# Optimization experiments

Hardware: AMD Instinct MI355X
Metric: run time of the kernel (lower is better)

## Reference

```python
import jax, jax.numpy as jnp
import numpy as np

B, S, F, D, H, L = 32, 512, 40, 512, 8, 4
T = S + 1
DK, DV = D // 2, D          # expand_k=0.5, expand_v=1.0 (fla GLA defaults)
HK, HV = DK // H, DV // H
GLR = 16                    # gate low-rank dim
GLN = 16.0                  # gate logit normalizer
MLP = 4 * D


def sin_pos(t, d, n=10000.0):
    pos = jnp.arange(t, dtype=jnp.float32)[:, None]
    den = jnp.power(n, 2.0 * jnp.arange(d // 2, dtype=jnp.float32) / d)
    e = jnp.zeros((t, d), jnp.float32)
    e = e.at[:, 0::2].set(jnp.sin(pos / den))
    e = e.at[:, 1::2].set(jnp.cos(pos / den))
    return e


def layernorm(x, w, b, eps=1e-5):
    m = x.mean(-1, keepdims=True)
    v = ((x - m) ** 2).mean(-1, keepdims=True)
    return (x - m) * jax.lax.rsqrt(v + eps) * w + b


def bin_norm(x, l1, b1, l2, b2, y1, y2):
    # x: (b, f, s). BiN: temporal z-norm with per-feature affine (X2) +
    # feature z-norm with per-time affine (X1); unbiased std, small std -> 1.
    st = jnp.sqrt(x.var(axis=2, ddof=1, keepdims=True))
    st = jnp.where(st < 1e-4, 1.0, st)
    Z2 = (x - x.mean(axis=2, keepdims=True)) / st
    X2 = l2[None, :, None] * Z2 + b2[None, :, None]
    sf = jnp.sqrt(x.var(axis=1, ddof=1, keepdims=True))
    sf = jnp.where(sf < 1e-4, 1.0, sf)
    Z1 = (x - x.mean(axis=1, keepdims=True)) / sf
    X1 = l1[None, None, :] * Z1 + b1[None, None, :]
    return y1 * X1 + y2 * X2


def gla_attn(x, qw, kw, vw, gw, gkw1, gkw2, gkb2, gnw, ow):
    # Gated linear attention, recurrent form: S_t = exp(gk_t) * S_{t-1} + k_t v_t^T
    b, t, _ = x.shape
    q = (x @ qw).reshape(b, t, H, HK) * (HK ** -0.5)
    k = (x @ kw).reshape(b, t, H, HK)
    v = (x @ vw).reshape(b, t, H, HV)
    g = (x @ gw).reshape(b, t, H, HV)
    gk = (jax.nn.log_sigmoid((x @ gkw1) @ gkw2 + gkb2) / GLN).reshape(b, t, H, HK)

    def step(Sc, inp):
        qt, kt, vt, gt = inp                       # (b,H,HK),(b,H,HK),(b,H,HV),(b,H,HK)
        Sc = Sc * jnp.exp(gt)[..., None] + kt[..., None] * vt[..., None, :]
        return Sc, jnp.einsum('bhk,bhkv->bhv', qt, Sc)

    init = jnp.zeros((b, H, HK, HV), x.dtype)
    to_t = lambda a: jnp.swapaxes(a, 0, 1)        # (t, b, H, dim)
    _, o = jax.lax.scan(step, init, (to_t(q), to_t(k), to_t(v), to_t(gk)))
    o = jnp.swapaxes(o, 0, 1)                     # (b, t, H, HV)
    o = o * jax.lax.rsqrt((o * o).mean(-1, keepdims=True) + 1e-5) * gnw  # head RMSNorm
    o = o * g * jax.nn.sigmoid(g)                 # swish output gate
    return o.reshape(b, t, DV) @ ow


def setup_inputs():
    key = jax.random.key(0)
    ks = iter(jax.random.split(key, 64))
    r = lambda shape, s=0.02: jax.random.normal(next(ks), shape, jnp.float32) * s
    return dict(
        x=jax.random.normal(next(ks), (B, S, F), jnp.float32),
        bin_l1=r((S,), 0.1), bin_b1=jnp.zeros((S,), jnp.float32),
        bin_l2=r((F,), 0.1), bin_b2=jnp.zeros((F,), jnp.float32),
        bin_y1=jnp.float32(0.5), bin_y2=jnp.float32(0.5),
        emb_w=r((F, D)), emb_b=jnp.zeros((D,), jnp.float32),
        cls_token=jnp.zeros((D,), jnp.float32),
        ln1_w=jnp.ones((L, D), jnp.float32), ln1_b=jnp.zeros((L, D), jnp.float32),
        q_w=r((L, D, DK)), k_w=r((L, D, DK)), v_w=r((L, D, DV)), g_w=r((L, D, DV)),
        gk_w1=r((L, D, GLR)), gk_w2=r((L, GLR, DK)), gk_b2=jnp.zeros((L, DK), jnp.float32),
        gnorm_w=jnp.ones((L, HV), jnp.float32),
        o_w=r((L, DV, D)),
        ln2_w=jnp.ones((L, D), jnp.float32), ln2_b=jnp.zeros((L, D), jnp.float32),
        mlp_w1=r((L, D, MLP)), mlp_b1=jnp.zeros((L, MLP), jnp.float32),
        mlp_w2=r((L, MLP, D)), mlp_b2=jnp.zeros((L, D), jnp.float32),
        head_w=r((D, 3)), head_b=jnp.zeros((3,), jnp.float32),
    )


def reference(x, bin_l1, bin_b1, bin_l2, bin_b2, bin_y1, bin_y2, emb_w, emb_b,
              cls_token, ln1_w, ln1_b, q_w, k_w, v_w, g_w, gk_w1, gk_w2, gk_b2,
              gnorm_w, o_w, ln2_w, ln2_b, mlp_w1, mlp_b1, mlp_w2, mlp_b2,
              head_w, head_b):
    h = bin_norm(jnp.swapaxes(x, 1, 2), bin_l1, bin_b1, bin_l2, bin_b2, bin_y1, bin_y2)
    h = jnp.swapaxes(h, 1, 2) @ emb_w + emb_b                    # (b, s, D)
    cls = jnp.broadcast_to(cls_token, (h.shape[0], 1, D))
    h = jnp.concatenate([h, cls], axis=1) + sin_pos(T, D)[None]  # (b, s+1, D)
    for i in range(L):
        a = gla_attn(layernorm(h, ln1_w[i], ln1_b[i]), q_w[i], k_w[i], v_w[i],
                     g_w[i], gk_w1[i], gk_w2[i], gk_b2[i], gnorm_w[i], o_w[i])
        h = h + a
        m = layernorm(h, ln2_w[i], ln2_b[i])
        m = jax.nn.gelu(m @ mlp_w1[i] + mlp_b1[i], approximate=False)
        h = h + m @ mlp_w2[i] + mlp_b2[i]
    return h[:, -1] @ head_w + head_b                            # (b, 3)
```

## Files before the change

kernel.cpp:

```cpp
#include <hip/hip_runtime.h>
#include <hip/hip_bf16.h>
#include <hip/hip_fp16.h>
#include <math.h>

#define Bsz   32
#define Ssz   512
#define Fsz   40
#define Dsz   512
#define Hh    8
#define Lnum  4
#define Tsz   513
#define DKsz  256
#define DVsz  512
#define HKsz  32
#define HVsz  64
#define Msz   (Bsz*Tsz)
#define Mpad  16512
#define MLPsz 2048
#define NCH   16
#define CSZ   33
#define QKVG  1536
#define VOFF  8404992

typedef __attribute__((ext_vector_type(4))) float f32x4;
typedef __attribute__((ext_vector_type(8))) short bf16x8;

__device__ __forceinline__ float bf2f(short s) {
  unsigned int u = ((unsigned int)(unsigned short)s) << 16;
  return __builtin_bit_cast(float, u);
}
__device__ __forceinline__ short f2bf(float f) {
  __hip_bfloat16 b = __float2bfloat16(f);
  return __builtin_bit_cast(short, b);
}

__device__ __forceinline__ float wave_sum(float v) {
#pragma unroll
  for (int off = 32; off > 0; off >>= 1) v += __shfl_xor(v, off, 64);
  return v;
}

__global__ void pos_kernel(float* __restrict__ pos) {
  int idx = blockIdx.x * 256 + threadIdx.x;
  if (idx >= Tsz * Dsz) return;
  int t = idx / Dsz, d = idx % Dsz;
  float e = (float)(2 * (d >> 1)) / (float)Dsz;
  float den = powf(10000.f, e);
  float a = (float)t / den;
  pos[idx] = (d & 1) ? cosf(a) : sinf(a);
}

__global__ void tstat_kernel(const float* __restrict__ x,
                             float* __restrict__ mt, float* __restrict__ rst) {
  int bf = blockIdx.x;
  int b = bf / Fsz, f = bf % Fsz;
  int lane = threadIdx.x;
  const float* xp = x + (size_t)b * Ssz * Fsz + f;
  float s = 0.f, sq = 0.f;
  for (int i = lane; i < Ssz; i += 64) {
    float v = xp[(size_t)i * Fsz];
    s += v; sq += v * v;
  }
  s = wave_sum(s); sq = wave_sum(sq);
  if (lane == 0) {
    float m = s / (float)Ssz;
    float var = (sq - (float)Ssz * m * m) / (float)(Ssz - 1);
    float st = sqrtf(fmaxf(var, 0.f));
    if (st < 1e-4f) st = 1.f;
    mt[bf] = m;
    rst[bf] = 1.f / st;
  }
}

__global__ __launch_bounds__(64) void binorm_kernel(
    const float* __restrict__ x, const float* __restrict__ l1,
    const float* __restrict__ b1, const float* __restrict__ l2,
    const float* __restrict__ b2, const float* __restrict__ y1p,
    const float* __restrict__ y2p, const float* __restrict__ mt,
    const float* __restrict__ rst, float* __restrict__ xbT) {
  int row = blockIdx.x;
  int lane = threadIdx.x;
  int b = row / Tsz, t = row % Tsz;
  bool valid = (row < Msz) && (t < Ssz);
  if (!valid) {
    if (lane < Fsz) xbT[(size_t)lane * Mpad + row] = 0.f;
    return;
  }
  float xv = 0.f;
  const float* xp = x + ((size_t)b * Ssz + t) * Fsz;
  if (lane < Fsz) xv = xp[lane];
  float s  = wave_sum(lane < Fsz ? xv : 0.f);
  float sq = wave_sum(lane < Fsz ? xv * xv : 0.f);
  float m = s / (float)Fsz;
  float var = (sq - (float)Fsz * m * m) / (float)(Fsz - 1);
  float sf = sqrtf(fmaxf(var, 0.f));
  if (sf < 1e-4f) sf = 1.f;
  if (lane < Fsz) {
    float y1 = y1p[0], y2 = y2p[0];
    float z1 = (xv - m) / sf;
    float X1 = l1[t] * z1 + b1[t];
    int bf = b * Fsz + lane;
    float z2 = (xv - mt[bf]) * rst[bf];
    float X2 = l2[lane] * z2 + b2[lane];
    xbT[(size_t)lane * Mpad + row] = y1 * X1 + y2 * X2;
  }
}

__global__ __launch_bounds__(256, 4) void embgemm_kernel(
    const float* __restrict__ xbT, const float* __restrict__ emb_w,
    const float* __restrict__ emb_b, const float* __restrict__ cls,
    const float* __restrict__ pos, float* __restrict__ h) {
  __shared__ float as[Fsz][64];
  __shared__ float bs[Fsz][64];
  int tid = threadIdx.x, tx = tid & 15, ty = tid >> 4;
  int r0 = blockIdx.x * 64, c0 = blockIdx.y * 64;
  for (int idx = tid; idx < Fsz * 64; idx += 256) {
    int f = idx >> 6, r = idx & 63;
    as[f][r] = xbT[(size_t)f * Mpad + r0 + r];
    bs[f][r] = emb_w[f * Dsz + c0 + r];
  }
  __syncthreads();
  float acc[4][4] = {};
#pragma unroll 5
  for (int f = 0; f < Fsz; ++f) {
    float4 a = *(const float4*)&as[f][ty * 4];
    float4 bv = *(const float4*)&bs[f][tx * 4];
    float av[4] = {a.x, a.y, a.z, a.w};
    float bw[4] = {bv.x, bv.y, bv.z, bv.w};
#pragma unroll
    for (int i = 0; i < 4; ++i)
#pragma unroll
      for (int j = 0; j < 4; ++j) acc[i][j] += av[i] * bw[j];
  }
#pragma unroll
  for (int i = 0; i < 4; ++i) {
    int gm = r0 + ty * 4 + i;
    int t = gm % Tsz;
    const float* pp = pos + (size_t)t * Dsz;
    bool iscls = (t == Ssz);
    int gn = c0 + tx * 4;
#pragma unroll
    for (int j = 0; j < 4; ++j) {
      float v = iscls ? (cls[gn + j] + pp[gn + j])
                      : (acc[i][j] + emb_b[gn + j] + pp[gn + j]);
      h[(size_t)gm * Dsz + gn + j] = v;
    }
  }
}

__global__ __launch_bounds__(64) void ln_kernel(
    const float* __restrict__ in, const float* __restrict__ w,
    const float* __restrict__ b, short* __restrict__ out) {
  int row = blockIdx.x, lane = threadIdx.x;
  const float* p = in + (size_t)row * Dsz;
  float4 v0 = *(const float4*)(p + lane * 8);
  float4 v1 = *(const float4*)(p + lane * 8 + 4);
  float s  = v0.x + v0.y + v0.z + v0.w + v1.x + v1.y + v1.z + v1.w;
  float sq = v0.x*v0.x + v0.y*v0.y + v0.z*v0.z + v0.w*v0.w
           + v1.x*v1.x + v1.y*v1.y + v1.z*v1.z + v1.w*v1.w;
  s = wave_sum(s); sq = wave_sum(sq);
  float m = s * (1.f / Dsz);
  float var = sq * (1.f / Dsz) - m * m;
  float r = rsqrtf(var + 1e-5f);
  float4 w0 = *(const float4*)(w + lane * 8);
  float4 w1 = *(const float4*)(w + lane * 8 + 4);
  float4 b0 = *(const float4*)(b + lane * 8);
  float4 b1v = *(const float4*)(b + lane * 8 + 4);
  bf16x8 pk;
  pk[0] = f2bf((v0.x - m) * r * w0.x + b0.x);
  pk[1] = f2bf((v0.y - m) * r * w0.y + b0.y);
  pk[2] = f2bf((v0.z - m) * r * w0.z + b0.z);
  pk[3] = f2bf((v0.w - m) * r * w0.w + b0.w);
  pk[4] = f2bf((v1.x - m) * r * w1.x + b1v.x);
  pk[5] = f2bf((v1.y - m) * r * w1.y + b1v.y);
  pk[6] = f2bf((v1.z - m) * r * w1.z + b1v.z);
  pk[7] = f2bf((v1.w - m) * r * w1.w + b1v.w);
  *(bf16x8*)(out + (size_t)row * Dsz + lane * 8) = pk;
}

__global__ __launch_bounds__(256) void wt_kernel(const float* __restrict__ W,
    short* __restrict__ Wt, int K, int N) {
  __shared__ float t[32][33];
  int k0 = blockIdx.x * 32, n0 = blockIdx.y * 32;
  int tx = threadIdx.x & 31, ty = threadIdx.x >> 5;
#pragma unroll
  for (int r = 0; r < 32; r += 8)
    t[ty + r][tx] = W[(size_t)(k0 + ty + r) * N + n0 + tx];
  __syncthreads();
#pragma unroll
  for (int r = 0; r < 32; r += 8)
    Wt[(size_t)(n0 + ty + r) * K + k0 + tx] = f2bf(t[tx][ty + r]);
}

__global__ __launch_bounds__(256) void wt4_kernel(const float* __restrict__ qw,
    const float* __restrict__ kw, const float* __restrict__ vw,
    const float* __restrict__ gw, short* __restrict__ Wt) {
  __shared__ float t[32][33];
  int k0 = blockIdx.x * 32, n0g = blockIdx.y * 32;
  const float* W; int n0, ld;
  if (n0g < 256)       { W = qw; n0 = n0g;        ld = DKsz; }
  else if (n0g < 512)  { W = kw; n0 = n0g - 256;  ld = DKsz; }
  else if (n0g < 1024) { W = vw; n0 = n0g - 512;  ld = DVsz; }
  else                 { W = gw; n0 = n0g - 1024; ld = DVsz; }
  int tx = threadIdx.x & 31, ty = threadIdx.x >> 5;
#pragma unroll
  for (int r = 0; r < 32; r += 8)
    t[ty + r][tx] = W[(size_t)(k0 + ty + r) * ld + n0 + tx];
  __syncthreads();
#pragma unroll
  for (int r = 0; r < 32; r += 8)
    Wt[(size_t)(n0g + ty + r) * Dsz + k0 + tx] = f2bf(t[tx][ty + r]);
}

template<int ACT, int OBF, int SCAT>
__global__ __launch_bounds__(256) void mgemm_kernel(
    const short* __restrict__ A, const short* __restrict__ Bt,
    void* __restrict__ Cv, const float* __restrict__ bias,
    const float* __restrict__ resid, int N, int K) {
  __shared__ short As[128 * 64];
  __shared__ short Bs[128 * 64];
  int tid = threadIdx.x;
  int lane = tid & 63, wid = tid >> 6;
  int wr = wid >> 1, wc = wid & 1;
  int m0 = blockIdx.x * 128, n0 = blockIdx.y * 128;
  f32x4 acc[4][4];
#pragma unroll
  for (int i = 0; i < 4; ++i)
#pragma unroll
    for (int j = 0; j < 4; ++j) acc[i][j] = (f32x4){0.f, 0.f, 0.f, 0.f};

  int kq = lane >> 4;
  int rsel = lane & 15;

  for (int kt = 0; kt < K; kt += 64) {
#pragma unroll
    for (int i = 0; i < 4; ++i) {
      int li = i * 256 + tid;
      int row = li >> 3;
      int gsrc = (li & 7) ^ (row & 7);
      const short* ga = A + (size_t)(m0 + row) * K + kt + gsrc * 8;
      const short* gb = Bt + (size_t)(n0 + row) * K + kt + gsrc * 8;
      int base = (i * 256 + wid * 64) * 8;
      __builtin_amdgcn_global_load_lds(
          (const __attribute__((address_space(1))) unsigned int*)ga,
          (__attribute__((address_space(3))) unsigned int*)&As[base], 16, 0, 0);
      __builtin_amdgcn_global_load_lds(
          (const __attribute__((address_space(1))) unsigned int*)gb,
          (__attribute__((address_space(3))) unsigned int*)&Bs[base], 16, 0, 0);
    }
    __syncthreads();
#pragma unroll
    for (int s = 0; s < 2; ++s) {
      bf16x8 af[4], bfr[4];
#pragma unroll
      for (int i = 0; i < 4; ++i) {
        int row = wr * 64 + i * 16 + rsel;
        int slot = (s * 4 + kq) ^ (row & 7);
        af[i] = *(const bf16x8*)&As[row * 64 + slot * 8];
        int col = wc * 64 + i * 16 + rsel;
        int slotB = (s * 4 + kq) ^ (col & 7);
        bfr[i] = *(const bf16x8*)&Bs[col * 64 + slotB * 8];
      }
#pragma unroll
      for (int i = 0; i < 4; ++i)
#pragma unroll
        for (int j = 0; j < 4; ++j)
          acc[i][j] = __builtin_amdgcn_mfma_f32_16x16x32_bf16(af[i], bfr[j], acc[i][j], 0, 0, 0);
    }
    __syncthreads();
  }

#pragma unroll
  for (int i = 0; i < 4; ++i) {
    int rbase = m0 + wr * 64 + i * 16 + (lane >> 4) * 4;
#pragma unroll
    for (int j = 0; j < 4; ++j) {
      int gn = n0 + wc * 64 + j * 16 + (lane & 15);
      float bv = (SCAT == 0 && bias) ? bias[gn] : 0.f;
#pragma unroll
      for (int r = 0; r < 4; ++r) {
        int gm = rbase + r;
        float v = acc[i][j][r] + bv;
        if (SCAT == 0) {
          if (ACT == 1) v = 0.5f * v * (1.f + erff(v * 0.70710678118654752f));
          if (resid) v += resid[(size_t)gm * N + gn];
          if (OBF) ((short*)Cv)[(size_t)gm * N + gn] = f2bf(v);
          else     ((float*)Cv)[(size_t)gm * N + gn] = v;
        } else {
          if (gm < Msz) {
            int bq = gm / Tsz, tq = gm - bq * Tsz;
            if (gn < 512) {
              int hq = (gn >> 5) & 7;
              int off = (gn & 31) | ((gn & 256) >> 3);
              ((float*)Cv)[(((size_t)bq * 8 + hq) * Tsz + tq) * 64 + off] = v;
            } else if (gn < 1024) {
              int hq = (gn >> 6) & 7;
              ((float*)Cv)[(size_t)VOFF + (((size_t)bq * 8 + hq) * Tsz + tq) * 64 + (gn & 63)] = v;
            } else {
              int hq = (gn >> 6) & 7;
              ((__half*)const_cast<float*>(resid))[(((size_t)bq * 8 + hq) * Tsz + tq) * 64 + (gn & 63)] = __float2half(v);
            }
          }
        }
      }
    }
  }
}

__global__ __launch_bounds__(64) void gk1_kernel(const short* __restrict__ xn,
    const float* __restrict__ w1, float* __restrict__ gk1) {
  int m = blockIdx.x, lane = threadIdx.x;
  __shared__ float xr[512];
  bf16x8 v = *(const bf16x8*)(xn + (size_t)m * Dsz + lane * 8);
#pragma unroll
  for (int e = 0; e < 8; ++e) xr[lane * 8 + e] = bf2f(v[e]);
  __syncthreads();
  int c = lane & 15, q = lane >> 4;
  float acc = 0.f;
#pragma unroll 8
  for (int i = 0; i < 128; ++i) {
    int k = q * 128 + i;
    acc += xr[k] * w1[k * 16 + c];
  }
  acc += __shfl_xor(acc, 16, 64);
  acc += __shfl_xor(acc, 32, 64);
  if (lane < 16) gk1[(size_t)m * 16 + c] = acc;
}

__global__ __launch_bounds__(256) void gk2_kernel(
    const float* __restrict__ gk1, const float* __restrict__ w2,
    const float* __restrict__ b2, float* __restrict__ gkeP) {
  int m = blockIdx.x, n = threadIdx.x;
  __shared__ float row[16];
  if (n < 16) row[n] = gk1[(size_t)m * 16 + n];
  __syncthreads();
  float acc = b2[n];
#pragma unroll
  for (int kk = 0; kk < 16; ++kk) acc += row[kk] * w2[kk * 256 + n];
  float z = acc;
  float ls = (z >= 0.f) ? -log1pf(expf(-z)) : z - log1pf(expf(z));
  int b = m / Tsz, t = m - b * Tsz;
  int h = n >> 5;
  gkeP[(((size_t)b * 8 + h) * Tsz + t) * 32 + (n & 31)] = expf(ls * 0.0625f);
}

__global__ __launch_bounds__(64) void scanA_kernel(
    const float* __restrict__ qkP, const float* __restrict__ gkeP,
    float* __restrict__ Ac, float* __restrict__ Bc) {
  int gid = blockIdx.x;
  int bh = gid >> 4, c = gid & 15;
  int lane = threadIdx.x;
  int t0 = c * CSZ;
  int nst = min(CSZ, Tsz - t0);
  __shared__ __align__(16) float s_k[CSZ * 32];
  __shared__ __align__(16) float s_g[CSZ * 32];
  __shared__ __align__(16) float s_v[CSZ * 64];
  const size_t rowbase = (size_t)bh * Tsz + t0;
  const float* qksrc = qkP + rowbase * 64;
  const float* vsrc  = qkP + (size_t)VOFF + rowbase * 64;
  const float* gsrc  = gkeP + rowbase * 32;
  int nkg = nst * 8;
#pragma unroll
  for (int i = 0; i < 5; ++i) {
    int gi = i * 64 + lane;
    if (gi < nkg) {
      int st = gi >> 3, g4 = (gi & 7) * 4;
      __builtin_amdgcn_global_load_lds(
        (const __attribute__((address_space(1))) unsigned int*)(qksrc + (size_t)st * 64 + 32 + g4),
        (__attribute__((address_space(3))) unsigned int*)s_k + i * 256, 16, 0, 0);
      __builtin_amdgcn_global_load_lds(
        (const __attribute__((address_space(1))) unsigned int*)(gsrc + (size_t)gi * 4),
        (__attribute__((address_space(3))) unsigned int*)s_g + i * 256, 16, 0, 0);
    }
  }
  int nv = nst * 16;
#pragma unroll
  for (int i = 0; i < 9; ++i) {
    int gi = i * 64 + lane;
    if (gi < nv)
      __builtin_amdgcn_global_load_lds(
        (const __attribute__((address_space(1))) unsigned int*)(vsrc + (size_t)gi * 4),
        (__attribute__((address_space(3))) unsigned int*)s_v + i * 256, 16, 0, 0);
  }
  float S[32];
#pragma unroll
  for (int i = 0; i < 32; ++i) S[i] = 0.f;
  float ac = 1.f;
  __syncthreads();
  for (int ts = 0; ts < nst; ++ts) {
    float vv = s_v[ts * 64 + lane];
#pragma unroll
    for (int j = 0; j < 8; ++j) {
      float4 kk = *(const float4*)&s_k[ts * 32 + j * 4];
      float4 gg = *(const float4*)&s_g[ts * 32 + j * 4];
      S[4*j+0] = S[4*j+0] * gg.x + kk.x * vv;
      S[4*j+1] = S[4*j+1] * gg.y + kk.y * vv;
      S[4*j+2] = S[4*j+2] * gg.z + kk.z * vv;
      S[4*j+3] = S[4*j+3] * gg.w + kk.w * vv;
    }
    ac *= s_g[ts * 32 + (lane & 31)];
  }
  float* bp = Bc + ((size_t)gid * 64 + lane) * 32;
#pragma unroll
  for (int j = 0; j < 8; ++j)
    *(float4*)(bp + j * 4) = make_float4(S[4*j+0], S[4*j+1], S[4*j+2], S[4*j+3]);
  if (lane < 32) Ac[(size_t)gid * 32 + lane] = ac;
}

__global__ __launch_bounds__(64) void scanB_kernel(
    const float* __restrict__ Ac, float* __restrict__ Bc) {
  int bh = blockIdx.x;
  int lane = threadIdx.x;
  float cur[32];
#pragma unroll
  for (int i = 0; i < 32; ++i) cur[i] = 0.f;
  __shared__ float sA[32];
  for (int c = 0; c < NCH; ++c) {
    size_t gid = (size_t)bh * NCH + c;
    float* bp = Bc + (gid * 64 + lane) * 32;
    __syncthreads();
    if (lane < 32) sA[lane] = Ac[gid * 32 + lane];
    __syncthreads();
    float4 tb[8];
#pragma unroll
    for (int j = 0; j < 8; ++j) tb[j] = *(const float4*)(bp + j * 4);
#pragma unroll
    for (int j = 0; j < 8; ++j)
      *(float4*)(bp + j * 4) = make_float4(cur[4*j+0], cur[4*j+1], cur[4*j+2], cur[4*j+3]);
#pragma unroll
    for (int j = 0; j < 8; ++j) {
      cur[4*j+0] = sA[4*j+0] * cur[4*j+0] + tb[j].x;
      cur[4*j+1] = sA[4*j+1] * cur[4*j+1] + tb[j].y;
      cur[4*j+2] = sA[4*j+2] * cur[4*j+2] + tb[j].z;
      cur[4*j+3] = sA[4*j+3] * cur[4*j+3] + tb[j].w;
    }
  }
}

__global__ __launch_bounds__(64) void scanC_kernel(
    const float* __restrict__ qkP, const __half* __restrict__ gP,
    const float* __restrict__ gkeP, const float* __restrict__ gnw,
    const float* __restrict__ Bc, short* __restrict__ att) {
  int gid = blockIdx.x;
  int bh = gid >> 4, c = gid & 15;
  int b = bh >> 3, hh = bh & 7;
  int lane = threadIdx.x;
  int t0 = c * CSZ;
  int nst = min(CSZ, Tsz - t0);
  __shared__ __align__(16) float s_qk[CSZ * 64];
  __shared__ __align__(16) float s_g[CSZ * 32];
  __shared__ __align__(16) float s_v[CSZ * 64];
  __shared__ __align__(16) __half s_gt[CSZ * 64];
  const size_t rowbase = (size_t)bh * Tsz + t0;
  const float* qksrc = qkP + rowbase * 64;
  const float* vsrc  = qkP + (size_t)VOFF + rowbase * 64;
  const float* gsrc  = gkeP + rowbase * 32;
  const __half* gtsrc = gP + rowbase * 64;
  int n16 = nst * 16;
#pragma unroll
  for (int i = 0; i < 9; ++i) {
    int gi = i * 64 + lane;
    if (gi < n16) {
      __builtin_amdgcn_global_load_lds(
        (const __attribute__((address_space(1))) unsigned int*)(qksrc + (size_t)gi * 4),
        (__attribute__((address_space(3))) unsigned int*)s_qk + i * 256, 16, 0, 0);
      __builtin_amdgcn_global_load_lds(
        (const __attribute__((address_space(1))) unsigned int*)(vsrc + (size_t)gi * 4),
        (__attribute__((address_space(3))) unsigned int*)s_v + i * 256, 16, 0, 0);
    }
  }
  int n8 = nst * 8;
#pragma unroll
  for (int i = 0; i < 5; ++i) {
    int gi = i * 64 + lane;
    if (gi < n8) {
      __builtin_amdgcn_global_load_lds(
        (const __attribute__((address_space(1))) unsigned int*)(gsrc + (size_t)gi * 4),
        (__attribute__((address_space(3))) unsigned int*)s_g + i * 256, 16, 0, 0);
      __builtin_amdgcn_global_load_lds(
        (const __attribute__((address_space(1))) unsigned int*)((const unsigned int*)gtsrc + (size_t)gi * 4),
        (__attribute__((address_space(3))) unsigned int*)s_gt + i * 256, 16, 0, 0);
    }
  }
  float S[32];
  const float* sp = Bc + ((size_t)gid * 64 + lane) * 32;
#pragma unroll
  for (int j = 0; j < 8; ++j) {
    float4 sv4 = *(const float4*)(sp + j * 4);
    S[4*j+0] = sv4.x; S[4*j+1] = sv4.y; S[4*j+2] = sv4.z; S[4*j+3] = sv4.w;
  }
  float gn = gnw[lane];
  __syncthreads();
  for (int ts = 0; ts < nst; ++ts) {
    float vv = s_v[ts * 64 + lane];
    float gv = __half2float(s_gt[ts * 64 + lane]);
    float o = 0.f;
#pragma unroll
    for (int j = 0; j < 8; ++j) {
      float4 qq = *(const float4*)&s_qk[ts * 64 + j * 4];
      float4 kk = *(const float4*)&s_qk[ts * 64 + 32 + j * 4];
      float4 gg = *(const float4*)&s_g[ts * 32 + j * 4];
      S[4*j+0] = S[4*j+0] * gg.x + kk.x * vv;  o += qq.x * S[4*j+0];
      S[4*j+1] = S[4*j+1] * gg.y + kk.y * vv;  o += qq.y * S[4*j+1];
      S[4*j+2] = S[4*j+2] * gg.z + kk.z * vv;  o += qq.z * S[4*j+2];
      S[4*j+3] = S[4*j+3] * gg.w + kk.w * vv;  o += qq.w * S[4*j+3];
    }
    o *= 0.17677669529663689f;
    float ss = wave_sum(o * o);
    float r = rsqrtf(ss * (1.f / 64.f) + 1e-5f);
    float sig = 1.f / (1.f + expf(-gv));
    att[((size_t)b * Tsz + t0 + ts) * DVsz + hh * HVsz + lane] = f2bf(o * r * gn * gv * sig);
  }
}

__global__ __launch_bounds__(64) void head_kernel(
    const float* __restrict__ h, const float* __restrict__ hw,
    const float* __restrict__ hb, float* __restrict__ out) {
  int b = blockIdx.x, lane = threadIdx.x;
  const float* p = h + ((size_t)b * Tsz + Ssz) * Dsz;
  float p0 = 0.f, p1 = 0.f, p2 = 0.f;
#pragma unroll
  for (int j = 0; j < 8; ++j) {
    int d = lane + j * 64;
    float hv = p[d];
    p0 += hv * hw[d * 3 + 0];
    p1 += hv * hw[d * 3 + 1];
    p2 += hv * hw[d * 3 + 2];
  }
  p0 = wave_sum(p0); p1 = wave_sum(p1); p2 = wave_sum(p2);
  if (lane == 0) {
    out[b * 3 + 0] = p0 + hb[0];
    out[b * 3 + 1] = p1 + hb[1];
    out[b * 3 + 2] = p2 + hb[2];
  }
}

extern "C" void kernel_launch(void* const* d_in, const int* in_sizes, int n_in,
                              void* d_out, int out_size, void* d_ws, size_t ws_size,
                              hipStream_t stream) {
  const float* x       = (const float*)d_in[0];
  const float* bin_l1  = (const float*)d_in[1];
  const float* bin_b1  = (const float*)d_in[2];
  const float* bin_l2  = (const float*)d_in[3];
  const float* bin_b2  = (const float*)d_in[4];
  const float* bin_y1  = (const float*)d_in[5];
  const float* bin_y2  = (const float*)d_in[6];
  const float* emb_w   = (const float*)d_in[7];
  const float* emb_b   = (const float*)d_in[8];
  const float* cls     = (const float*)d_in[9];
  const float* ln1_w   = (const float*)d_in[10];
  const float* ln1_b   = (const float*)d_in[11];
  const float* q_w     = (const float*)d_in[12];
  const float* k_w     = (const float*)d_in[13];
  const float* v_w     = (const float*)d_in[14];
  const float* g_w     = (const float*)d_in[15];
  const float* gk_w1   = (const float*)d_in[16];
  const float* gk_w2   = (const float*)d_in[17];
  const float* gk_b2   = (const float*)d_in[18];
  const float* gnorm_w = (const float*)d_in[19];
  const float* o_w     = (const float*)d_in[20];
  const float* ln2_w   = (const float*)d_in[21];
  const float* ln2_b   = (const float*)d_in[22];
  const float* mlp_w1  = (const float*)d_in[23];
  const float* mlp_b1  = (const float*)d_in[24];
  const float* mlp_w2  = (const float*)d_in[25];
  const float* mlp_b2  = (const float*)d_in[26];
  const float* head_w  = (const float*)d_in[27];
  const float* head_b  = (const float*)d_in[28];
  float* out = (float*)d_out;

  char* wptr = (char*)d_ws;
  auto alloc = [&](size_t bytes) { char* p = wptr; wptr += (bytes + 255) & ~(size_t)255; return p; };
  float* pos  = (float*)alloc((size_t)Tsz * Dsz * 4);
  float* h    = (float*)alloc((size_t)Mpad * Dsz * 4);
  short* xn   = (short*)alloc((size_t)Mpad * Dsz * 2);
  float* qkP  = (float*)alloc((size_t)Mpad * MLPsz * 2);
  float* gkeP = (float*)alloc((size_t)256 * Tsz * 32 * 4);
  __half* gP  = (__half*)alloc((size_t)256 * Tsz * 64 * 2);
  float* gk1b = (float*)alloc((size_t)Mpad * 16 * 4);
  float* mt   = (float*)alloc((size_t)Bsz * Fsz * 4);
  float* rst  = (float*)alloc((size_t)Bsz * Fsz * 4);
  float* Ac   = (float*)alloc((size_t)Bsz * Hh * NCH * 32 * 4);
  float* Bc   = (float*)alloc((size_t)Bsz * Hh * NCH * 64 * 32 * 4);
  short* wtr  = (short*)alloc((size_t)3145728 * 2);
  float* xbT  = qkP;
  short* mid  = (short*)qkP;
  short* att  = xn;

  short* qkvT = wtr;
  short* owT  = qkvT + 786432;
  short* m1T  = owT + 262144;
  short* m2T  = m1T + 1048576;

  hipLaunchKernelGGL(pos_kernel, dim3((Tsz * Dsz + 255) / 256), dim3(256), 0, stream, pos);
  hipLaunchKernelGGL(tstat_kernel, dim3(Bsz * Fsz), dim3(64), 0, stream, x, mt, rst);
  hipLaunchKernelGGL(binorm_kernel, dim3(Mpad), dim3(64), 0, stream,
                     x, bin_l1, bin_b1, bin_l2, bin_b2, bin_y1, bin_y2, mt, rst, xbT);
  hipLaunchKernelGGL(embgemm_kernel, dim3(258, 8), dim3(256), 0, stream,
                     xbT, emb_w, emb_b, cls, pos, h);

  dim3 blk256(256);
  for (int l = 0; l < Lnum; ++l) {
    hipLaunchKernelGGL(wt4_kernel, dim3(16, 48), blk256, 0, stream,
                       q_w + (size_t)l*Dsz*DKsz, k_w + (size_t)l*Dsz*DKsz,
                       v_w + (size_t)l*Dsz*DVsz, g_w + (size_t)l*Dsz*DVsz, qkvT);
    hipLaunchKernelGGL(wt_kernel, dim3(16, 16), blk256, 0, stream, o_w   + (size_t)l*DVsz*Dsz,  owT, DVsz, Dsz);
    hipLaunchKernelGGL(wt_kernel, dim3(16, 64), blk256, 0, stream, mlp_w1+ (size_t)l*Dsz*MLPsz, m1T, Dsz, MLPsz);
    hipLaunchKernelGGL(wt_kernel, dim3(64, 16), blk256, 0, stream, mlp_w2+ (size_t)l*MLPsz*Dsz, m2T, MLPsz, Dsz);

    const float* lw1 = ln1_w + l * Dsz;  const float* lb1 = ln1_b + l * Dsz;
    const float* g1w = gk_w1 + (size_t)l * Dsz * 16;
    const float* g2w = gk_w2 + (size_t)l * 16 * DKsz;
    const float* g2b = gk_b2 + (size_t)l * DKsz;
    const float* gnw = gnorm_w + l * HVsz;
    const float* lw2 = ln2_w + l * Dsz;  const float* lb2 = ln2_b + l * Dsz;
    const float* m1b = mlp_b1 + (size_t)l * MLPsz;
    const float* m2b = mlp_b2 + (size_t)l * Dsz;

    hipLaunchKernelGGL(ln_kernel, dim3(Msz), dim3(64), 0, stream, h, lw1, lb1, xn);

    hipLaunchKernelGGL((mgemm_kernel<0,0,1>), dim3(129, 12), blk256, 0, stream,
                       xn, qkvT, (void*)qkP, (const float*)nullptr, (const float*)gP, QKVG, Dsz);
    hipLaunchKernelGGL(gk1_kernel, dim3(Msz), dim3(64), 0, stream, xn, g1w, gk1b);
    hipLaunchKernelGGL(gk2_kernel, dim3(Msz), blk256, 0, stream, gk1b, g2w, g2b, gkeP);

    hipLaunchKernelGGL(scanA_kernel, dim3(Bsz * Hh * NCH), dim3(64), 0, stream,
                       qkP, gkeP, Ac, Bc);
    hipLaunchKernelGGL(scanB_kernel, dim3(Bsz * Hh), dim3(64), 0, stream, Ac, Bc);
    hipLaunchKernelGGL(scanC_kernel, dim3(Bsz * Hh * NCH), dim3(64), 0, stream,
                       qkP, gP, gkeP, gnw, Bc, att);

    hipLaunchKernelGGL((mgemm_kernel<0,0,0>), dim3(129, 4), blk256, 0, stream,
                       att, owT, (void*)h, (const float*)nullptr, h, Dsz, DVsz);

    hipLaunchKernelGGL(ln_kernel, dim3(Msz), dim3(64), 0, stream, h, lw2, lb2, xn);
    hipLaunchKernelGGL((mgemm_kernel<1,1,0>), dim3(129, 16), blk256, 0, stream,
                       xn, m1T, (void*)mid, m1b, (const float*)nullptr, MLPsz, Dsz);
    hipLaunchKernelGGL((mgemm_kernel<0,0,0>), dim3(129, 4), blk256, 0, stream,
                       mid, m2T, (void*)h, m2b, h, Dsz, MLPsz);
  }

  hipLaunchKernelGGL(head_kernel, dim3(Bsz), dim3(64), 0, stream, h, head_w, head_b, out);
}
```

Baseline: 1.805 ms.

## Fold low-rank gate projection into QKVG GEMM and swap grid order

Precomputes the product gk_w1 @ gk_w2 into 256 extra bf16 rows of the transposed QKVG weight, so the gate logits come out of the main MFMA GEMM. The epilogue applies the bias, log-sigmoid and exp and writes gkeP directly, which removes the two per-row gk1/gk2 kernels and their launches. All GEMM launches also swap grid axes so consecutive blocks walk N for the same M tile, which may improve L2 reuse of the A rows. The cost is a wider GEMM (1792 columns), plus bf16 rounding of the merged gate weight and a rank-512 multiply that replaces the rank-16 path.

```diff
diff --git a/kernel.cpp b/kernel.cpp
--- a/kernel.cpp
+++ b/kernel.cpp
@@ -19,7 +19,7 @@
 #define MLPsz 2048
 #define NCH   16
 #define CSZ   33
-#define QKVG  1536
+#define QKVG2 1792
 #define VOFF  8404992
 
 typedef __attribute__((ext_vector_type(4))) float f32x4;
@@ -212,17 +212,34 @@
     Wt[(size_t)(n0g + ty + r) * Dsz + k0 + tx] = f2bf(t[tx][ty + r]);
 }
 
+__global__ __launch_bounds__(256) void gkw_kernel(const float* __restrict__ w1,
+    const float* __restrict__ w2, short* __restrict__ qkvT) {
+  int n = blockIdx.x;
+  int tid = threadIdx.x;
+  __shared__ float s2[16];
+  if (tid < 16) s2[tid] = w2[tid * 256 + n];
+  __syncthreads();
+#pragma unroll
+  for (int kk = 0; kk < 2; ++kk) {
+    int k = tid + kk * 256;
+    float acc = 0.f;
+#pragma unroll
+    for (int r = 0; r < 16; ++r) acc += w1[k * 16 + r] * s2[r];
+    qkvT[(size_t)(1536 + n) * Dsz + k] = f2bf(acc);
+  }
+}
+
 template<int ACT, int OBF, int SCAT>
 __global__ __launch_bounds__(256) void mgemm_kernel(
     const short* __restrict__ A, const short* __restrict__ Bt,
     void* __restrict__ Cv, const float* __restrict__ bias,
-    const float* __restrict__ resid, int N, int K) {
+    const float* __restrict__ resid, float* __restrict__ gkeP, int N, int K) {
   __shared__ short As[128 * 64];
   __shared__ short Bs[128 * 64];
   int tid = threadIdx.x;
   int lane = tid & 63, wid = tid >> 6;
   int wr = wid >> 1, wc = wid & 1;
-  int m0 = blockIdx.x * 128, n0 = blockIdx.y * 128;
+  int n0 = blockIdx.x * 128, m0 = blockIdx.y * 128;
   f32x4 acc[4][4];
 #pragma unroll
   for (int i = 0; i < 4; ++i)
@@ -296,52 +313,21 @@
             } else if (gn < 1024) {
               int hq = (gn >> 6) & 7;
               ((float*)Cv)[(size_t)VOFF + (((size_t)bq * 8 + hq) * Tsz + tq) * 64 + (gn & 63)] = v;
-            } else {
+            } else if (gn < 1536) {
               int hq = (gn >> 6) & 7;
               ((__half*)const_cast<float*>(resid))[(((size_t)bq * 8 + hq) * Tsz + tq) * 64 + (gn & 63)] = __float2half(v);
+            } else {
+              int gg = gn - 1536;
+              float z = v + bias[gg];
+              float ls = (z >= 0.f) ? -log1pf(expf(-z)) : z - log1pf(expf(z));
+              int hq = gg >> 5;
+              gkeP[(((size_t)bq * 8 + hq) * Tsz + tq) * 32 + (gg & 31)] = expf(ls * 0.0625f);
             }
           }
         }
       }
     }
   }
-}
-
-__global__ __launch_bounds__(64) void gk1_kernel(const short* __restrict__ xn,
-    const float* __restrict__ w1, float* __restrict__ gk1) {
-  int m = blockIdx.x, lane = threadIdx.x;
-  __shared__ float xr[512];
-  bf16x8 v = *(const bf16x8*)(xn + (size_t)m * Dsz + lane * 8);
-#pragma unroll
-  for (int e = 0; e < 8; ++e) xr[lane * 8 + e] = bf2f(v[e]);
-  __syncthreads();
-  int c = lane & 15, q = lane >> 4;
-  float acc = 0.f;
-#pragma unroll 8
-  for (int i = 0; i < 128; ++i) {
-    int k = q * 128 + i;
-    acc += xr[k] * w1[k * 16 + c];
-  }
-  acc += __shfl_xor(acc, 16, 64);
-  acc += __shfl_xor(acc, 32, 64);
-  if (lane < 16) gk1[(size_t)m * 16 + c] = acc;
-}
-
-__global__ __launch_bounds__(256) void gk2_kernel(
-    const float* __restrict__ gk1, const float* __restrict__ w2,
-    const float* __restrict__ b2, float* __restrict__ gkeP) {
-  int m = blockIdx.x, n = threadIdx.x;
-  __shared__ float row[16];
-  if (n < 16) row[n] = gk1[(size_t)m * 16 + n];
-  __syncthreads();
-  float acc = b2[n];
-#pragma unroll
-  for (int kk = 0; kk < 16; ++kk) acc += row[kk] * w2[kk * 256 + n];
-  float z = acc;
-  float ls = (z >= 0.f) ? -log1pf(expf(-z)) : z - log1pf(expf(z));
-  int b = m / Tsz, t = m - b * Tsz;
-  int h = n >> 5;
-  gkeP[(((size_t)b * 8 + h) * Tsz + t) * 32 + (n & 31)] = expf(ls * 0.0625f);
 }
 
 __global__ __launch_bounds__(64) void scanA_kernel(
@@ -577,18 +563,17 @@
   float* qkP  = (float*)alloc((size_t)Mpad * MLPsz * 2);
   float* gkeP = (float*)alloc((size_t)256 * Tsz * 32 * 4);
   __half* gP  = (__half*)alloc((size_t)256 * Tsz * 64 * 2);
-  float* gk1b = (float*)alloc((size_t)Mpad * 16 * 4);
   float* mt   = (float*)alloc((size_t)Bsz * Fsz * 4);
   float* rst  = (float*)alloc((size_t)Bsz * Fsz * 4);
   float* Ac   = (float*)alloc((size_t)Bsz * Hh * NCH * 32 * 4);
   float* Bc   = (float*)alloc((size_t)Bsz * Hh * NCH * 64 * 32 * 4);
-  short* wtr  = (short*)alloc((size_t)3145728 * 2);
+  short* wtr  = (short*)alloc((size_t)3276800 * 2);
   float* xbT  = qkP;
   short* mid  = (short*)qkP;
   short* att  = xn;
 
   short* qkvT = wtr;
-  short* owT  = qkvT + 786432;
+  short* owT  = qkvT + 917504;
   short* m1T  = owT + 262144;
   short* m2T  = m1T + 1048576;
 
@@ -604,13 +589,13 @@
     hipLaunchKernelGGL(wt4_kernel, dim3(16, 48), blk256, 0, stream,
                        q_w + (size_t)l*Dsz*DKsz, k_w + (size_t)l*Dsz*DKsz,
                        v_w + (size_t)l*Dsz*DVsz, g_w + (size_t)l*Dsz*DVsz, qkvT);
+    hipLaunchKernelGGL(gkw_kernel, dim3(256), blk256, 0, stream,
+                       gk_w1 + (size_t)l*Dsz*16, gk_w2 + (size_t)l*16*DKsz, qkvT);
     hipLaunchKernelGGL(wt_kernel, dim3(16, 16), blk256, 0, stream, o_w   + (size_t)l*DVsz*Dsz,  owT, DVsz, Dsz);
     hipLaunchKernelGGL(wt_kernel, dim3(16, 64), blk256, 0, stream, mlp_w1+ (size_t)l*Dsz*MLPsz, m1T, Dsz, MLPsz);
     hipLaunchKernelGGL(wt_kernel, dim3(64, 16), blk256, 0, stream, mlp_w2+ (size_t)l*MLPsz*Dsz, m2T, MLPsz, Dsz);
 
     const float* lw1 = ln1_w + l * Dsz;  const float* lb1 = ln1_b + l * Dsz;
-    const float* g1w = gk_w1 + (size_t)l * Dsz * 16;
-    const float* g2w = gk_w2 + (size_t)l * 16 * DKsz;
     const float* g2b = gk_b2 + (size_t)l * DKsz;
     const float* gnw = gnorm_w + l * HVsz;
     const float* lw2 = ln2_w + l * Dsz;  const float* lb2 = ln2_b + l * Dsz;
@@ -619,10 +604,8 @@
 
     hipLaunchKernelGGL(ln_kernel, dim3(Msz), dim3(64), 0, stream, h, lw1, lb1, xn);
 
-    hipLaunchKernelGGL((mgemm_kernel<0,0,1>), dim3(129, 12), blk256, 0, stream,
-                       xn, qkvT, (void*)qkP, (const float*)nullptr, (const float*)gP, QKVG, Dsz);
-    hipLaunchKernelGGL(gk1_kernel, dim3(Msz), dim3(64), 0, stream, xn, g1w, gk1b);
-    hipLaunchKernelGGL(gk2_kernel, dim3(Msz), blk256, 0, stream, gk1b, g2w, g2b, gkeP);
+    hipLaunchKernelGGL((mgemm_kernel<0,0,1>), dim3(14, 129), blk256, 0, stream,
+                       xn, qkvT, (void*)qkP, g2b, (const float*)gP, gkeP, QKVG2, Dsz);
 
     hipLaunchKernelGGL(scanA_kernel, dim3(Bsz * Hh * NCH), dim3(64), 0, stream,
                        qkP, gkeP, Ac, Bc);
@@ -630,14 +613,14 @@
     hipLaunchKernelGGL(scanC_kernel, dim3(Bsz * Hh * NCH), dim3(64), 0, stream,
                        qkP, gP, gkeP, gnw, Bc, att);
 
-    hipLaunchKernelGGL((mgemm_kernel<0,0,0>), dim3(129, 4), blk256, 0, stream,
-                       att, owT, (void*)h, (const float*)nullptr, h, Dsz, DVsz);
+    hipLaunchKernelGGL((mgemm_kernel<0,0,0>), dim3(4, 129), blk256, 0, stream,
+                       att, owT, (void*)h, (const float*)nullptr, h, (float*)nullptr, Dsz, DVsz);
 
     hipLaunchKernelGGL(ln_kernel, dim3(Msz), dim3(64), 0, stream, h, lw2, lb2, xn);
-    hipLaunchKernelGGL((mgemm_kernel<1,1,0>), dim3(129, 16), blk256, 0, stream,
-                       xn, m1T, (void*)mid, m1b, (const float*)nullptr, MLPsz, Dsz);
-    hipLaunchKernelGGL((mgemm_kernel<0,0,0>), dim3(129, 4), blk256, 0, stream,
-                       mid, m2T, (void*)h, m2b, h, Dsz, MLPsz);
+    hipLaunchKernelGGL((mgemm_kernel<1,1,0>), dim3(16, 129), blk256, 0, stream,
+                       xn, m1T, (void*)mid, m1b, (const float*)nullptr, (float*)nullptr, MLPsz, Dsz);
+    hipLaunchKernelGGL((mgemm_kernel<0,0,0>), dim3(4, 129), blk256, 0, stream,
+                       mid, m2T, (void*)h, m2b, h, (float*)nullptr, Dsz, MLPsz);
   }
 
   hipLaunchKernelGGL(head_kernel, dim3(Bsz), dim3(64), 0, stream, h, head_w, head_b, out);
```

Measured after the change: 2.481 ms. 1.37x slower.
